# Performance work log

Hardware: AMD Instinct MI355X
Metric: run time of the kernel (lower is better)

Reference implementation:

```python
import jax, jax.numpy as jnp
import numpy as np

B, S, E = 2, 2048, 2048
KV, QPG, HD = 4, 4, 128  # 16 total heads, head_size=128
ROPE_THETA = 10000.0


def _rope_cos_sin(seq_len, head_size, dtype):
    inv_freq = 1.0 / (ROPE_THETA ** (jnp.arange(0, head_size, 2, dtype=jnp.float32) / head_size))
    pos = jnp.arange(seq_len, dtype=jnp.float32)
    freqs = pos[:, None] * inv_freq[None, :]            # [S, HD/2]
    emb = jnp.concatenate([freqs, freqs], axis=-1)       # [S, HD]
    return jnp.cos(emb).astype(dtype), jnp.sin(emb).astype(dtype)


def _rotate_half(x):
    x1, x2 = jnp.split(x, 2, axis=-1)
    return jnp.concatenate([-x2, x1], axis=-1)


def _apply_rope(x, cos, sin):
    # x: [..., S, HD]; cos/sin: [S, HD]
    return x * cos + _rotate_half(x) * sin


def setup_inputs() -> dict:
    key = jax.random.key(0)
    ks = jax.random.split(key, 8)
    scale = 0.02
    return {
        "x": jax.random.normal(ks[0], (B, S, E), jnp.float32),
        "wq": jax.random.normal(ks[1], (KV, QPG, HD, E), jnp.float32) * scale,
        "bq": jax.random.normal(ks[2], (KV, QPG, HD), jnp.float32) * scale,
        "wk": jax.random.normal(ks[3], (KV, HD, E), jnp.float32) * scale,
        "bk": jax.random.normal(ks[4], (KV, HD), jnp.float32) * scale,
        "wv": jax.random.normal(ks[5], (KV, HD, E), jnp.float32) * scale,
        "bv": jax.random.normal(ks[6], (KV, HD), jnp.float32) * scale,
        "wo": jax.random.normal(ks[7], (E, E), jnp.float32) * scale,
    }


def reference(x, wq, bq, wk, bk, wv, bv, wo):
    # QKV projections (out_first linear: y = W x + b)
    q = jnp.einsum('bse,kghe->bkgsh', x, wq) + bq[None, :, :, None, :]   # [B,KV,QPG,S,HD]
    k = jnp.einsum('bse,khe->bksh', x, wk) + bk[None, :, None, :]        # [B,KV,S,HD]
    v = jnp.einsum('bse,khe->bksh', x, wv) + bv[None, :, None, :]        # [B,KV,S,HD]

    cos, sin = _rope_cos_sin(S, HD, x.dtype)
    q = _apply_rope(q, cos, sin)
    k = _apply_rope(k, cos, sin)

    # GQA scaled dot-product attention with causal mask
    scale = 1.0 / jnp.sqrt(jnp.asarray(HD, x.dtype))
    scores = jnp.einsum('bkgsh,bkth->bkgst', q, k) * scale               # [B,KV,QPG,S,S]
    causal = jnp.tril(jnp.ones((S, S), dtype=bool))
    scores = jnp.where(causal, scores, jnp.asarray(-1e9, scores.dtype))
    att = jax.nn.softmax(scores, axis=-1)
    out = jnp.einsum('bkgst,bkth->bkgsh', att, v)                        # [B,KV,QPG,S,HD]

    # flatten (kv_heads, q_heads_per_group, head_size) -> heads*head_size and project
    out = out.transpose(0, 3, 1, 2, 4).reshape(B, S, KV * QPG * HD)      # [B,S,E]
    return jnp.einsum('bsf,ef->bse', out, wo)
```

## Files before the change

kernel.cpp:

```cpp
#include <hip/hip_runtime.h>

typedef unsigned short u16;
typedef short s16x8 __attribute__((ext_vector_type(8)));
typedef float f32x4 __attribute__((ext_vector_type(4)));
typedef float f32x16 __attribute__((ext_vector_type(16)));

__device__ __forceinline__ u16 f2bf(float f) {
  union { float f; unsigned u; } x; x.f = f;
  unsigned r = (x.u + 0x7fffu + ((x.u >> 16) & 1u)) >> 16;
  return (u16)r;
}
__device__ __forceinline__ unsigned bfbits_t(float f) {
  union { float f; unsigned u; } x; x.f = f;
  return x.u >> 16;
}
__device__ __forceinline__ float bf2f(u16 u) {
  union { unsigned u; float f; } x; x.u = ((unsigned)u) << 16;
  return x.f;
}

__device__ __forceinline__ void load_lds16(const u16* g, void* lds) {
  __builtin_amdgcn_global_load_lds(
      (const __attribute__((address_space(1))) unsigned int*)g,
      (__attribute__((address_space(3))) unsigned int*)lds, 16, 0, 0);
}

__global__ __launch_bounds__(256) void prep_kernel(
    const float* __restrict__ x,
    const float* __restrict__ wq, const float* __restrict__ wk,
    const float* __restrict__ wv,
    const float* __restrict__ bq, const float* __restrict__ bk,
    const float* __restrict__ bv,
    const float* __restrict__ wo,
    u16* __restrict__ xb, u16* __restrict__ wqkv,
    float* __restrict__ bqkv, u16* __restrict__ wob,
    float* __restrict__ cosb, float* __restrict__ sinb) {
  const int R0 = 2097152;
  const int R1 = R0 + 1572864;
  const int R2 = R1 + 1048576;
  const int R3 = R2 + 768;
  const int R4 = R3 + 131072;
  for (int id = blockIdx.x * 256 + threadIdx.x; id < R4; id += gridDim.x * 256) {
    if (id < R0) {
      float4 v = ((const float4*)x)[id];
      u16* d = xb + (size_t)id * 4;
      d[0] = f2bf(v.x); d[1] = f2bf(v.y); d[2] = f2bf(v.z); d[3] = f2bf(v.w);
    } else if (id < R1) {
      int g = id - R0;
      int row = g >> 9, c4 = (g & 511) * 4;
      const float* src; int srow;
      if (row < 2048)      { src = wq; srow = row; }
      else if (row < 2560) { src = wk; srow = row - 2048; }
      else                 { src = wv; srow = row - 2560; }
      float4 v = *(const float4*)&src[(size_t)srow * 2048 + c4];
      u16* d = wqkv + (size_t)row * 2048 + c4;
      d[0] = f2bf(v.x); d[1] = f2bf(v.y); d[2] = f2bf(v.z); d[3] = f2bf(v.w);
    } else if (id < R2) {
      int g = id - R1;
      float4 v = ((const float4*)wo)[g];
      u16* d = wob + (size_t)g * 4;
      d[0] = f2bf(v.x); d[1] = f2bf(v.y); d[2] = f2bf(v.z); d[3] = f2bf(v.w);
    } else if (id < R3) {
      int g4 = (id - R2) * 4;
      float4 v;
      if (g4 < 2048)      v = *(const float4*)&bq[g4];
      else if (g4 < 2560) v = *(const float4*)&bk[g4 - 2048];
      else                v = *(const float4*)&bv[g4 - 2560];
      *(float4*)&bqkv[g4] = v;
    } else {
      int g = id - R3;
      int s = g >> 6, i = g & 63;
      float freq = powf(10000.0f, -(float)i / 64.0f);
      float ang = (float)s * freq;
      cosb[g] = cosf(ang);
      sinb[g] = sinf(ang);
    }
  }
}

__global__ __launch_bounds__(256) void rope_all_kernel(u16* __restrict__ Qb,
                                                       u16* __restrict__ Kbuf,
                                                       const float* __restrict__ cosb,
                                                       const float* __restrict__ sinb) {
  const int total = (32 + 8) * 2048 * 64;
  for (int id = blockIdx.x * 256 + threadIdx.x; id < total; id += gridDim.x * 256) {
    int i = id & 63;
    int rs = id >> 6;
    int s = rs & 2047;
    u16* p;
    size_t base;
    if (rs < 65536) { p = Qb;   base = (size_t)rs * 128; }
    else            { p = Kbuf; base = (size_t)(rs - 65536) * 128; }
    float x1 = bf2f(p[base + i]);
    float x2 = bf2f(p[base + i + 64]);
    float c = cosb[s * 64 + i], sn = sinb[s * 64 + i];
    p[base + i]      = f2bf(x1 * c - x2 * sn);
    p[base + i + 64] = f2bf(x2 * c + x1 * sn);
  }
}

__global__ __launch_bounds__(256) void transpose_v_kernel(const u16* __restrict__ V,
                                                          u16* __restrict__ Vt) {
  __shared__ u16 tile[64][130];
  const int t = threadIdx.x;
  const int hb = blockIdx.x, s0 = blockIdx.y * 64;
  const u16* src = V + ((size_t)hb * 2048 + s0) * 128;
#pragma unroll
  for (int i = 0; i < 4; ++i) {
    int c = i * 256 + t;
    int s = c >> 4, d8 = (c & 15) * 8;
    *(s16x8*)&tile[s][d8] = *(const s16x8*)&src[(size_t)s * 128 + d8];
  }
  __syncthreads();
  u16* dst = Vt + (size_t)hb * 128 * 2048 + s0;
#pragma unroll
  for (int i = 0; i < 4; ++i) {
    int c = i * 256 + t;
    int d = c & 127, s8 = (c >> 7) * 8;
    s16x8 v;
#pragma unroll
    for (int e = 0; e < 8; ++e) v[e] = (short)tile[s8 + e][d];
    *(s16x8*)&dst[(size_t)d * 2048 + s8] = v;
  }
}

__global__ __launch_bounds__(512) void gemm_bt_kernel(
    const u16* __restrict__ A, const u16* __restrict__ Bw,
    const float* __restrict__ bias,
    float* __restrict__ C, int ldc,
    u16* __restrict__ Qp, u16* __restrict__ Kp, u16* __restrict__ Vp,
    int M, int N, int K, int mode) {
  __shared__ u16 sA[128 * 64];
  __shared__ u16 sB[128 * 64];
  const int t = threadIdx.x;
  const int w = t >> 6, l = t & 63;
  const int lg = l >> 4, lr = l & 15;
  const int wm = (w >> 2) * 64, wn = (w & 3) * 32;
  const int m0 = blockIdx.y * 128, n0 = blockIdx.x * 128;

  f32x4 acc[4][2];
#pragma unroll
  for (int i = 0; i < 4; ++i)
#pragma unroll
    for (int j = 0; j < 2; ++j)
#pragma unroll
      for (int r = 0; r < 4; ++r) acc[i][j][r] = 0.0f;

  for (int k0 = 0; k0 < K; k0 += 64) {
#pragma unroll
    for (int i = 0; i < 2; ++i) {
      int c = i * 512 + t;
      int row = c >> 3, cc = (c & 7) ^ (row & 7);
      load_lds16(A + (size_t)(m0 + row) * K + k0 + cc * 8,
                 (char*)sA + i * 8192 + w * 1024);
      load_lds16(Bw + (size_t)(n0 + row) * K + k0 + cc * 8,
                 (char*)sB + i * 8192 + w * 1024);
    }
    __syncthreads();
#pragma unroll
    for (int kc = 0; kc < 2; ++kc) {
      const int rch = (((kc * 4 + lg) ^ (lr & 7)) * 8);
      s16x8 af[4], bf[2];
#pragma unroll
      for (int m = 0; m < 4; ++m)
        af[m] = *(const s16x8*)&sA[(wm + m * 16 + lr) * 64 + rch];
#pragma unroll
      for (int n = 0; n < 2; ++n)
        bf[n] = *(const s16x8*)&sB[(wn + n * 16 + lr) * 64 + rch];
#pragma unroll
      for (int m = 0; m < 4; ++m)
#pragma unroll
        for (int n = 0; n < 2; ++n)
          acc[m][n] = __builtin_amdgcn_mfma_f32_16x16x32_bf16(af[m], bf[n], acc[m][n], 0, 0, 0);
    }
    __syncthreads();
  }

#pragma unroll
  for (int m = 0; m < 4; ++m) {
#pragma unroll
    for (int n = 0; n < 2; ++n) {
#pragma unroll
      for (int r = 0; r < 4; ++r) {
        int row = m0 + wm + m * 16 + (lg << 2) + r;
        int col = n0 + wn + n * 16 + lr;
        float val = acc[m][n][r];
        if (mode == 0) {
          val += bias[col];
          int b = row >> 11, s = row & 2047;
          u16 bvv = f2bf(val);
          if (col < 2048) {
            int h = col >> 7, d = col & 127;
            Qp[(((size_t)(b * 16 + h)) * 2048 + s) * 128 + d] = bvv;
          } else if (col < 2560) {
            int cc = col - 2048; int kh = cc >> 7, d = cc & 127;
            Kp[(((size_t)(b * 4 + kh)) * 2048 + s) * 128 + d] = bvv;
          } else {
            int cc = col - 2560; int kh = cc >> 7, d = cc & 127;
            Vp[(((size_t)(b * 4 + kh)) * 2048 + s) * 128 + d] = bvv;
          }
        } else {
          C[(size_t)row * ldc + col] = val;
        }
      }
    }
  }
}

__device__ const int PH_QC[16] = {7,-1, 7,0, 6,-1, 6,1, 5,-1, 5,2, 4,-1, 4,3};
__device__ const int PH_J0[16] = {0,0, 9,0, 0,0, 9,0, 0,0, 9,0, 0,0, 9,0};
__device__ const int PH_NT[16] = {9,0, 7,2, 9,0, 5,4, 9,0, 3,6, 9,0, 1,8};
__device__ const int PH_MD[16] = {1,0, 2,0, 1,0, 2,0, 1,0, 2,0, 1,0, 2,0};

__global__ __launch_bounds__(512) void flash_mfma_kernel(const u16* __restrict__ Q,
                                                         const u16* __restrict__ Kb,
                                                         const u16* __restrict__ Vtb,
                                                         u16* __restrict__ O,
                                                         u16* __restrict__ po,
                                                         float* __restrict__ pml) {
  const int S = 2048;
  __shared__ u16 sK[128 * 128];
  __shared__ u16 sVt[2 * 128 * 128];

  const int t = threadIdx.x, w = t >> 6, l = t & 63;
  const int l31 = l & 31, hi = l >> 5;
  const int bh = blockIdx.x, b = bh >> 4, h = bh & 15, kvh = h >> 2;
  const int slot = blockIdx.y;

  const u16* kbase = Kb + ((size_t)(b * 4 + kvh)) * S * 128;
  const u16* vtbase = Vtb + ((size_t)(b * 4 + kvh)) * 128 * S;

  const float C2 = 0.12753785f;

  auto stageK = [&](int kt) {
#pragma unroll
    for (int i = 0; i < 4; ++i) {
      int c = i * 512 + t;
      int j = c >> 4, cc = (c & 15) ^ (j & 15);
      load_lds16(kbase + ((size_t)(kt * 128 + j) * 128 + cc * 8),
                 (char*)sK + (i * 8192 + w * 1024));
    }
  };
  auto stageV = [&](int kt, int buf) {
#pragma unroll
    for (int i = 0; i < 4; ++i) {
      int c = i * 512 + t;
      int d = c >> 4, cc = (c & 15) ^ (d & 15);
      load_lds16(vtbase + ((size_t)d * S + kt * 128 + cc * 8),
                 (char*)sVt + buf * 32768 + (i * 8192 + w * 1024));
    }
  };

#pragma unroll 1
  for (int ph = 0; ph < 2; ++ph) {
    const int qc = PH_QC[slot * 2 + ph];
    const int ntc = PH_NT[slot * 2 + ph];
    if (ntc == 0) break;
    const int j0 = PH_J0[slot * 2 + ph];
    const int md = PH_MD[slot * 2 + ph];
    const int qw = qc * 256 + w * 32;
    const int q_glob = qw + l31;

    const u16* qbase = Q + ((size_t)bh * S + qw) * 128;
    s16x8 qb[8];
#pragma unroll
    for (int ks = 0; ks < 8; ++ks)
      qb[ks] = *(const s16x8*)&qbase[(size_t)l31 * 128 + ks * 16 + hi * 8];

    f32x16 o0, o1, o2, o3;
#pragma unroll
    for (int r = 0; r < 16; ++r) { o0[r] = 0.f; o1[r] = 0.f; o2[r] = 0.f; o3[r] = 0.f; }
    float mrun = -3e38f, lsum = 0.0f;

    stageV(j0, 0);
    stageK(j0);
    __syncthreads();

    int cur = 0;
    for (int kt2 = 0; kt2 < ntc; ++kt2) {
      const int kt = j0 + kt2;
      const bool act = (kt * 128 <= qw + 31);
      const bool more = (kt2 + 1 < ntc);

      if (more) stageV(kt + 1, cur ^ 1);

      f32x16 sc0, sc1, sc2, sc3;
      if (act) {
#pragma unroll
        for (int r = 0; r < 16; ++r) { sc0[r] = 0.f; sc1[r] = 0.f; sc2[r] = 0.f; sc3[r] = 0.f; }
        const int chkb = (l31 & 15);
        __builtin_amdgcn_s_setprio(1);
#pragma unroll
        for (int ks = 0; ks < 8; ++ks) {
          int chk = ((2 * ks + hi) ^ chkb) * 8;
          s16x8 kf0 = *(const s16x8*)&sK[(l31) * 128 + chk];
          s16x8 kf1 = *(const s16x8*)&sK[(32 + l31) * 128 + chk];
          s16x8 kf2 = *(const s16x8*)&sK[(64 + l31) * 128 + chk];
          s16x8 kf3 = *(const s16x8*)&sK[(96 + l31) * 128 + chk];
          sc0 = __builtin_amdgcn_mfma_f32_32x32x16_bf16(kf0, qb[ks], sc0, 0, 0, 0);
          sc1 = __builtin_amdgcn_mfma_f32_32x32x16_bf16(kf1, qb[ks], sc1, 0, 0, 0);
          sc2 = __builtin_amdgcn_mfma_f32_32x32x16_bf16(kf2, qb[ks], sc2, 0, 0, 0);
          sc3 = __builtin_amdgcn_mfma_f32_32x32x16_bf16(kf3, qb[ks], sc3, 0, 0, 0);
        }
        __builtin_amdgcn_s_setprio(0);
      }

      __syncthreads();

      if (more) stageK(kt + 1);

      if (act) {
        const u16* sVc = &sVt[cur * 16384];

        if (kt * 128 + 127 > qw) {
          const int j0m = kt * 128;
#pragma unroll
          for (int r = 0; r < 16; ++r) {
            int jr = j0m + (r & 3) + 8 * (r >> 2) + 4 * hi;
            sc0[r] = (jr <= q_glob) ? sc0[r] : -3e38f;
            sc1[r] = (jr + 32 <= q_glob) ? sc1[r] : -3e38f;
            sc2[r] = (jr + 64 <= q_glob) ? sc2[r] : -3e38f;
            sc3[r] = (jr + 96 <= q_glob) ? sc3[r] : -3e38f;
          }
        }

        float tm[16];
#pragma unroll
        for (int r = 0; r < 16; ++r)
          tm[r] = fmaxf(fmaxf(sc0[r], sc1[r]), fmaxf(sc2[r], sc3[r]));
#pragma unroll
        for (int s2 = 8; s2 >= 1; s2 >>= 1)
#pragma unroll
          for (int r = 0; r < s2; ++r) tm[r] = fmaxf(tm[r], tm[r + s2]);
        float mt = fmaxf(tm[0], __shfl_xor(tm[0], 32));
        float mt2 = mt * C2;
        bool resc = (mt2 > mrun + 8.0f);
        if (resc) {
          float Mn = mt2;
          float corr = exp2f(mrun - Mn);
          lsum *= corr;
#pragma unroll
          for (int r = 0; r < 16; ++r) {
            o0[r] *= corr; o1[r] *= corr; o2[r] *= corr; o3[r] *= corr;
          }
          mrun = Mn;
        }
        const float Mn = mrun;
        float lacc = 0.0f;

        {
          unsigned pk[16];
#pragma unroll
          for (int m = 0; m < 8; ++m) {
            float pa_ = exp2f(__builtin_fmaf(sc0[2 * m], C2, -Mn));
            float pb_ = exp2f(__builtin_fmaf(sc0[2 * m + 1], C2, -Mn));
            lacc += pa_ + pb_;
            pk[m] = (bfbits_t(pb_) << 16) | bfbits_t(pa_);
          }
#pragma unroll
          for (int m = 0; m < 8; ++m) {
            float pa_ = exp2f(__builtin_fmaf(sc1[2 * m], C2, -Mn));
            float pb_ = exp2f(__builtin_fmaf(sc1[2 * m + 1], C2, -Mn));
            lacc += pa_ + pb_;
            pk[8 + m] = (bfbits_t(pb_) << 16) | bfbits_t(pa_);
          }
          unsigned pkx[16];
#pragma unroll
          for (int i = 0; i < 16; ++i) pkx[i] = __shfl_xor(pk[i], 32);
          __builtin_amdgcn_s_setprio(1);
#pragma unroll
          for (int ks = 0; ks < 4; ++ks) {
            const int base = (ks >> 1) * 8 + 4 * (ks & 1);
            unsigned pw[4];
            pw[0] = hi ? pkx[base + 2] : pk[base + 0];
            pw[1] = hi ? pkx[base + 3] : pk[base + 1];
            pw[2] = hi ? pk[base + 2] : pkx[base + 0];
            pw[3] = hi ? pk[base + 3] : pkx[base + 1];
            s16x8 pa = *(const s16x8*)pw;
#pragma unroll
            for (int dt = 0; dt < 4; ++dt) {
              int d = dt * 32 + l31;
              s16x8 vt = *(const s16x8*)&sVc[d * 128 + (((2 * ks + hi) ^ (d & 15)) * 8)];
              if (dt == 0) o0 = __builtin_amdgcn_mfma_f32_32x32x16_bf16(vt, pa, o0, 0, 0, 0);
              if (dt == 1) o1 = __builtin_amdgcn_mfma_f32_32x32x16_bf16(vt, pa, o1, 0, 0, 0);
              if (dt == 2) o2 = __builtin_amdgcn_mfma_f32_32x32x16_bf16(vt, pa, o2, 0, 0, 0);
              if (dt == 3) o3 = __builtin_amdgcn_mfma_f32_32x32x16_bf16(vt, pa, o3, 0, 0, 0);
            }
          }
          __builtin_amdgcn_s_setprio(0);
        }

        {
          unsigned pk[16];
#pragma unroll
          for (int m = 0; m < 8; ++m) {
            float pa_ = exp2f(__builtin_fmaf(sc2[2 * m], C2, -Mn));
            float pb_ = exp2f(__builtin_fmaf(sc2[2 * m + 1], C2, -Mn));
            lacc += pa_ + pb_;
            pk[m] = (bfbits_t(pb_) << 16) | bfbits_t(pa_);
          }
#pragma unroll
          for (int m = 0; m < 8; ++m) {
            float pa_ = exp2f(__builtin_fmaf(sc3[2 * m], C2, -Mn));
            float pb_ = exp2f(__builtin_fmaf(sc3[2 * m + 1], C2, -Mn));
            lacc += pa_ + pb_;
            pk[8 + m] = (bfbits_t(pb_) << 16) | bfbits_t(pa_);
          }
          unsigned pkx[16];
#pragma unroll
          for (int i = 0; i < 16; ++i) pkx[i] = __shfl_xor(pk[i], 32);
          __builtin_amdgcn_s_setprio(1);
#pragma unroll
          for (int ks = 0; ks < 4; ++ks) {
            const int base = (ks >> 1) * 8 + 4 * (ks & 1);
            unsigned pw[4];
            pw[0] = hi ? pkx[base + 2] : pk[base + 0];
            pw[1] = hi ? pkx[base + 3] : pk[base + 1];
            pw[2] = hi ? pk[base + 2] : pkx[base + 0];
            pw[3] = hi ? pk[base + 3] : pkx[base + 1];
            s16x8 pa = *(const s16x8*)pw;
#pragma unroll
            for (int dt = 0; dt < 4; ++dt) {
              int d = dt * 32 + l31;
              s16x8 vt = *(const s16x8*)&sVc[d * 128 + (((8 + 2 * ks + hi) ^ (d & 15)) * 8)];
              if (dt == 0) o0 = __builtin_amdgcn_mfma_f32_32x32x16_bf16(vt, pa, o0, 0, 0, 0);
              if (dt == 1) o1 = __builtin_amdgcn_mfma_f32_32x32x16_bf16(vt, pa, o1, 0, 0, 0);
              if (dt == 2) o2 = __builtin_amdgcn_mfma_f32_32x32x16_bf16(vt, pa, o2, 0, 0, 0);
              if (dt == 3) o3 = __builtin_amdgcn_mfma_f32_32x32x16_bf16(vt, pa, o3, 0, 0, 0);
            }
          }
          __builtin_amdgcn_s_setprio(0);
        }
        lsum += lacc;
      }

      __syncthreads();
      cur ^= 1;
    }

    float ls = lsum + __shfl_xor(lsum, 32);
    float inv = (ls > 0.0f) ? 1.0f / ls : 0.0f;
    if (md == 0) {
      size_t obase = ((size_t)b * S + q_glob) * 2048 + h * 128;
#pragma unroll
      for (int dt = 0; dt < 4; ++dt) {
        const f32x16& ov = (dt == 0) ? o0 : (dt == 1) ? o1 : (dt == 2) ? o2 : o3;
#pragma unroll
        for (int g = 0; g < 4; ++g) {
          int d0 = dt * 32 + 8 * g + 4 * hi;
          unsigned u0 = (unsigned)f2bf(ov[4 * g] * inv) | ((unsigned)f2bf(ov[4 * g + 1] * inv) << 16);
          unsigned u1 = (unsigned)f2bf(ov[4 * g + 2] * inv) | ((unsigned)f2bf(ov[4 * g + 3] * inv) << 16);
          uint2 u; u.x = u0; u.y = u1;
          *(uint2*)&O[obase + d0] = u;
        }
      }
    } else {
      const int pid = ((bh << 2) + (qc - 4)) * 2 + (md - 1);
      const int qrow = w * 32 + l31;
      size_t pbase = (size_t)pid * 32768 + (size_t)qrow * 128;
#pragma unroll
      for (int dt = 0; dt < 4; ++dt) {
        const f32x16& ov = (dt == 0) ? o0 : (dt == 1) ? o1 : (dt == 2) ? o2 : o3;
#pragma unroll
        for (int g = 0; g < 4; ++g) {
          int d0 = dt * 32 + 8 * g + 4 * hi;
          unsigned u0 = (unsigned)f2bf(ov[4 * g] * inv) | ((unsigned)f2bf(ov[4 * g + 1] * inv) << 16);
          unsigned u1 = (unsigned)f2bf(ov[4 * g + 2] * inv) | ((unsigned)f2bf(ov[4 * g + 3] * inv) << 16);
          uint2 u; u.x = u0; u.y = u1;
          *(uint2*)&po[pbase + d0] = u;
        }
      }
      if (hi == 0) {
        pml[pid * 512 + qrow * 2]     = mrun;
        pml[pid * 512 + qrow * 2 + 1] = ls;
      }
    }
    if (ph == 0 && PH_NT[slot * 2 + 1] != 0) __syncthreads();
  }
}

__global__ __launch_bounds__(256) void flash_merge_kernel(const u16* __restrict__ po,
                                                          const float* __restrict__ pml,
                                                          u16* __restrict__ att) {
  const int t = threadIdx.x;
  const int tl = blockIdx.x >> 4;
  const int row = (blockIdx.x & 15) * 16 + (t >> 4);
  const int d8 = (t & 15) * 8;
  const int hh2 = tl >> 2, qc = (tl & 3) + 4;
  const int pid0 = tl * 2, pid1 = pid0 + 1;
  float m0 = pml[pid0 * 512 + row * 2], l0 = pml[pid0 * 512 + row * 2 + 1];
  float m1 = pml[pid1 * 512 + row * 2], l1 = pml[pid1 * 512 + row * 2 + 1];
  float M = fmaxf(m0, m1);
  float w0 = l0 * exp2f(m0 - M), w1 = l1 * exp2f(m1 - M);
  float inv = 1.0f / (w0 + w1);
  w0 *= inv; w1 *= inv;
  s16x8 a = *(const s16x8*)&po[(size_t)pid0 * 32768 + row * 128 + d8];
  s16x8 c = *(const s16x8*)&po[(size_t)pid1 * 32768 + row * 128 + d8];
  int b = hh2 >> 4, hh = hh2 & 15;
  size_t base = ((size_t)b * 2048 + qc * 256 + row) * 2048 + hh * 128 + d8;
  u16 outv[8];
#pragma unroll
  for (int e = 0; e < 8; ++e)
    outv[e] = f2bf(w0 * bf2f((u16)a[e]) + w1 * bf2f((u16)c[e]));
  *(s16x8*)&att[base] = *(const s16x8*)outv;
}


extern "C" void kernel_launch(void* const* d_in, const int* in_sizes, int n_in,
                              void* d_out, int out_size, void* d_ws, size_t ws_size,
                              hipStream_t stream) {
  const float* x  = (const float*)d_in[0];
  const float* wq = (const float*)d_in[1];
  const float* bq = (const float*)d_in[2];
  const float* wk = (const float*)d_in[3];
  const float* bk = (const float*)d_in[4];
  const float* wv = (const float*)d_in[5];
  const float* bv = (const float*)d_in[6];
  const float* wo = (const float*)d_in[7];
  float* out = (float*)d_out;

  char* ws = (char*)d_ws;
  u16* xb    = (u16*)ws;    ws += (size_t)4096 * 2048 * 2;
  u16* wqkv  = (u16*)ws;    ws += (size_t)3072 * 2048 * 2;
  float* bqkv = (float*)ws; ws += (size_t)3072 * 4;
  u16* wob   = (u16*)ws;    ws += (size_t)2048 * 2048 * 2;
  u16* Qb    = (u16*)ws;    ws += (size_t)32 * 2048 * 128 * 2;
  u16* Kbuf  = (u16*)ws;    ws += (size_t)8 * 2048 * 128 * 2;
  u16* Vbuf  = (u16*)ws;    ws += (size_t)8 * 2048 * 128 * 2;
  u16* Vt    = (u16*)ws;    ws += (size_t)8 * 128 * 2048 * 2;
  float* cosb = (float*)ws; ws += (size_t)2048 * 64 * 4;
  float* sinb = (float*)ws; ws += (size_t)2048 * 64 * 4;
  u16* att   = (u16*)ws;    ws += (size_t)4096 * 2048 * 2;

  u16* po = xb;
  float* pml = (float*)Vbuf;

  prep_kernel<<<2048, 256, 0, stream>>>(x, wq, wk, wv, bq, bk, bv, wo,
                                        xb, wqkv, bqkv, wob, cosb, sinb);

  gemm_bt_kernel<<<dim3(24, 32), 512, 0, stream>>>(xb, wqkv, bqkv, nullptr, 0,
                                                   Qb, Kbuf, Vbuf, 4096, 3072, 2048, 0);
  transpose_v_kernel<<<dim3(8, 32), 256, 0, stream>>>(Vbuf, Vt);
  rope_all_kernel<<<2048, 256, 0, stream>>>(Qb, Kbuf, cosb, sinb);

  flash_mfma_kernel<<<dim3(32, 8), 512, 0, stream>>>(Qb, Kbuf, Vt, att, po, pml);
  flash_merge_kernel<<<2048, 256, 0, stream>>>(po, pml, att);

  gemm_bt_kernel<<<dim3(16, 32), 512, 0, stream>>>(att, wob, nullptr, out, 2048,
                                                   nullptr, nullptr, nullptr, 4096, 2048, 2048, 1);
}
```

Baseline: 197.6 us.

## Split every query chunk into two KV halves and single-buffer V

New measurement: 226.0 us. 1.14x slower.

```diff
diff --git a/kernel.cpp b/kernel.cpp
--- a/kernel.cpp
+++ b/kernel.cpp
@@ -207,11 +207,6 @@
   }
 }
 
-__device__ const int PH_QC[16] = {7,-1, 7,0, 6,-1, 6,1, 5,-1, 5,2, 4,-1, 4,3};
-__device__ const int PH_J0[16] = {0,0, 9,0, 0,0, 9,0, 0,0, 9,0, 0,0, 9,0};
-__device__ const int PH_NT[16] = {9,0, 7,2, 9,0, 5,4, 9,0, 3,6, 9,0, 1,8};
-__device__ const int PH_MD[16] = {1,0, 2,0, 1,0, 2,0, 1,0, 2,0, 1,0, 2,0};
-
 __global__ __launch_bounds__(512) void flash_mfma_kernel(const u16* __restrict__ Q,
                                                          const u16* __restrict__ Kb,
                                                          const u16* __restrict__ Vtb,
@@ -220,17 +215,35 @@
                                                          float* __restrict__ pml) {
   const int S = 2048;
   __shared__ u16 sK[128 * 128];
-  __shared__ u16 sVt[2 * 128 * 128];
+  __shared__ u16 sVt[128 * 128];
 
   const int t = threadIdx.x, w = t >> 6, l = t & 63;
   const int l31 = l & 31, hi = l >> 5;
   const int bh = blockIdx.x, b = bh >> 4, h = bh & 15, kvh = h >> 2;
-  const int slot = blockIdx.y;
+  const int y = blockIdx.y;
+  const int piece = y >> 3;
+  const int qc = piece ? (y - 8) : (7 - y);
+  const int ntc = qc + 1;
+  const int j0 = piece ? (qc + 1) : 0;
 
   const u16* kbase = Kb + ((size_t)(b * 4 + kvh)) * S * 128;
   const u16* vtbase = Vtb + ((size_t)(b * 4 + kvh)) * 128 * S;
 
   const float C2 = 0.12753785f;
+
+  const int qw = qc * 256 + w * 32;
+  const int q_glob = qw + l31;
+
+  const u16* qbase = Q + ((size_t)bh * S + qw) * 128;
+  s16x8 qb[8];
+#pragma unroll
+  for (int ks = 0; ks < 8; ++ks)
+    qb[ks] = *(const s16x8*)&qbase[(size_t)l31 * 128 + ks * 16 + hi * 8];
+
+  f32x16 o0, o1, o2, o3;
+#pragma unroll
+  for (int r = 0; r < 16; ++r) { o0[r] = 0.f; o1[r] = 0.f; o2[r] = 0.f; o3[r] = 0.f; }
+  float mrun = -3e38f, lsum = 0.0f;
 
   auto stageK = [&](int kt) {
 #pragma unroll
@@ -241,241 +254,214 @@
                  (char*)sK + (i * 8192 + w * 1024));
     }
   };
-  auto stageV = [&](int kt, int buf) {
+  auto stageV = [&](int kt) {
 #pragma unroll
     for (int i = 0; i < 4; ++i) {
       int c = i * 512 + t;
       int d = c >> 4, cc = (c & 15) ^ (d & 15);
       load_lds16(vtbase + ((size_t)d * S + kt * 128 + cc * 8),
-                 (char*)sVt + buf * 32768 + (i * 8192 + w * 1024));
+                 (char*)sVt + (i * 8192 + w * 1024));
     }
   };
 
-#pragma unroll 1
-  for (int ph = 0; ph < 2; ++ph) {
-    const int qc = PH_QC[slot * 2 + ph];
-    const int ntc = PH_NT[slot * 2 + ph];
-    if (ntc == 0) break;
-    const int j0 = PH_J0[slot * 2 + ph];
-    const int md = PH_MD[slot * 2 + ph];
-    const int qw = qc * 256 + w * 32;
-    const int q_glob = qw + l31;
-
-    const u16* qbase = Q + ((size_t)bh * S + qw) * 128;
-    s16x8 qb[8];
-#pragma unroll
-    for (int ks = 0; ks < 8; ++ks)
-      qb[ks] = *(const s16x8*)&qbase[(size_t)l31 * 128 + ks * 16 + hi * 8];
-
-    f32x16 o0, o1, o2, o3;
-#pragma unroll
-    for (int r = 0; r < 16; ++r) { o0[r] = 0.f; o1[r] = 0.f; o2[r] = 0.f; o3[r] = 0.f; }
-    float mrun = -3e38f, lsum = 0.0f;
-
-    stageV(j0, 0);
-    stageK(j0);
+  stageK(j0);
+  stageV(j0);
+  __syncthreads();
+
+  for (int kt2 = 0; kt2 < ntc; ++kt2) {
+    const int kt = j0 + kt2;
+    const bool act = (kt * 128 <= qw + 31);
+    const bool more = (kt2 + 1 < ntc);
+
+    f32x16 sc0, sc1, sc2, sc3;
+    if (act) {
+#pragma unroll
+      for (int r = 0; r < 16; ++r) { sc0[r] = 0.f; sc1[r] = 0.f; sc2[r] = 0.f; sc3[r] = 0.f; }
+      const int chkb = (l31 & 15);
+      __builtin_amdgcn_s_setprio(1);
+#pragma unroll
+      for (int ks = 0; ks < 8; ++ks) {
+        int chk = ((2 * ks + hi) ^ chkb) * 8;
+        s16x8 kf0 = *(const s16x8*)&sK[(l31) * 128 + chk];
+        s16x8 kf1 = *(const s16x8*)&sK[(32 + l31) * 128 + chk];
+        s16x8 kf2 = *(const s16x8*)&sK[(64 + l31) * 128 + chk];
+        s16x8 kf3 = *(const s16x8*)&sK[(96 + l31) * 128 + chk];
+        sc0 = __builtin_amdgcn_mfma_f32_32x32x16_bf16(kf0, qb[ks], sc0, 0, 0, 0);
+        sc1 = __builtin_amdgcn_mfma_f32_32x32x16_bf16(kf1, qb[ks], sc1, 0, 0, 0);
+        sc2 = __builtin_amdgcn_mfma_f32_32x32x16_bf16(kf2, qb[ks], sc2, 0, 0, 0);
+        sc3 = __builtin_amdgcn_mfma_f32_32x32x16_bf16(kf3, qb[ks], sc3, 0, 0, 0);
+      }
+      __builtin_amdgcn_s_setprio(0);
+    }
+
     __syncthreads();
 
-    int cur = 0;
-    for (int kt2 = 0; kt2 < ntc; ++kt2) {
-      const int kt = j0 + kt2;
-      const bool act = (kt * 128 <= qw + 31);
-      const bool more = (kt2 + 1 < ntc);
-
-      if (more) stageV(kt + 1, cur ^ 1);
-
-      f32x16 sc0, sc1, sc2, sc3;
-      if (act) {
-#pragma unroll
-        for (int r = 0; r < 16; ++r) { sc0[r] = 0.f; sc1[r] = 0.f; sc2[r] = 0.f; sc3[r] = 0.f; }
-        const int chkb = (l31 & 15);
+    if (more) stageK(kt + 1);
+
+    if (act) {
+      if (kt * 128 + 127 > qw) {
+        const int j0m = kt * 128;
+#pragma unroll
+        for (int r = 0; r < 16; ++r) {
+          int jr = j0m + (r & 3) + 8 * (r >> 2) + 4 * hi;
+          sc0[r] = (jr <= q_glob) ? sc0[r] : -3e38f;
+          sc1[r] = (jr + 32 <= q_glob) ? sc1[r] : -3e38f;
+          sc2[r] = (jr + 64 <= q_glob) ? sc2[r] : -3e38f;
+          sc3[r] = (jr + 96 <= q_glob) ? sc3[r] : -3e38f;
+        }
+      }
+
+      float tm[16];
+#pragma unroll
+      for (int r = 0; r < 16; ++r)
+        tm[r] = fmaxf(fmaxf(sc0[r], sc1[r]), fmaxf(sc2[r], sc3[r]));
+#pragma unroll
+      for (int s2 = 8; s2 >= 1; s2 >>= 1)
+#pragma unroll
+        for (int r = 0; r < s2; ++r) tm[r] = fmaxf(tm[r], tm[r + s2]);
+      float mt = fmaxf(tm[0], __shfl_xor(tm[0], 32));
+      float mt2 = mt * C2;
+      bool resc = (mt2 > mrun + 8.0f);
+      if (resc) {
+        float Mn = mt2;
+        float corr = exp2f(mrun - Mn);
+        lsum *= corr;
+#pragma unroll
+        for (int r = 0; r < 16; ++r) {
+          o0[r] *= corr; o1[r] *= corr; o2[r] *= corr; o3[r] *= corr;
+        }
+        mrun = Mn;
+      }
+      const float Mn = mrun;
+      float lacc = 0.0f;
+
+      {
+        unsigned pk[16];
+#pragma unroll
+        for (int m = 0; m < 8; ++m) {
+          float pa_ = exp2f(__builtin_fmaf(sc0[2 * m], C2, -Mn));
+          float pb_ = exp2f(__builtin_fmaf(sc0[2 * m + 1], C2, -Mn));
+          lacc += pa_ + pb_;
+          pk[m] = (bfbits_t(pb_) << 16) | bfbits_t(pa_);
+        }
+#pragma unroll
+        for (int m = 0; m < 8; ++m) {
+          float pa_ = exp2f(__builtin_fmaf(sc1[2 * m], C2, -Mn));
+          float pb_ = exp2f(__builtin_fmaf(sc1[2 * m + 1], C2, -Mn));
+          lacc += pa_ + pb_;
+          pk[8 + m] = (bfbits_t(pb_) << 16) | bfbits_t(pa_);
+        }
+        unsigned pkx[16];
+#pragma unroll
+        for (int i = 0; i < 16; ++i) pkx[i] = __shfl_xor(pk[i], 32);
         __builtin_amdgcn_s_setprio(1);
 #pragma unroll
-        for (int ks = 0; ks < 8; ++ks) {
-          int chk = ((2 * ks + hi) ^ chkb) * 8;
-          s16x8 kf0 = *(const s16x8*)&sK[(l31) * 128 + chk];
-          s16x8 kf1 = *(const s16x8*)&sK[(32 + l31) * 128 + chk];
-          s16x8 kf2 = *(const s16x8*)&sK[(64 + l31) * 128 + chk];
-          s16x8 kf3 = *(const s16x8*)&sK[(96 + l31) * 128 + chk];
-          sc0 = __builtin_amdgcn_mfma_f32_32x32x16_bf16(kf0, qb[ks], sc0, 0, 0, 0);
-          sc1 = __builtin_amdgcn_mfma_f32_32x32x16_bf16(kf1, qb[ks], sc1, 0, 0, 0);
-          sc2 = __builtin_amdgcn_mfma_f32_32x32x16_bf16(kf2, qb[ks], sc2, 0, 0, 0);
-          sc3 = __builtin_amdgcn_mfma_f32_32x32x16_bf16(kf3, qb[ks], sc3, 0, 0, 0);
+        for (int ks = 0; ks < 4; ++ks) {
+          const int base = (ks >> 1) * 8 + 4 * (ks & 1);
+          unsigned pw[4];
+          pw[0] = hi ? pkx[base + 2] : pk[base + 0];
+          pw[1] = hi ? pkx[base + 3] : pk[base + 1];
+          pw[2] = hi ? pk[base + 2] : pkx[base + 0];
+          pw[3] = hi ? pk[base + 3] : pkx[base + 1];
+          s16x8 pa = *(const s16x8*)pw;
+#pragma unroll
+          for (int dt = 0; dt < 4; ++dt) {
+            int d = dt * 32 + l31;
+            s16x8 vt = *(const s16x8*)&sVt[d * 128 + (((2 * ks + hi) ^ (d & 15)) * 8)];
+            if (dt == 0) o0 = __builtin_amdgcn_mfma_f32_32x32x16_bf16(vt, pa, o0, 0, 0, 0);
+            if (dt == 1) o1 = __builtin_amdgcn_mfma_f32_32x32x16_bf16(vt, pa, o1, 0, 0, 0);
+            if (dt == 2) o2 = __builtin_amdgcn_mfma_f32_32x32x16_bf16(vt, pa, o2, 0, 0, 0);
+            if (dt == 3) o3 = __builtin_amdgcn_mfma_f32_32x32x16_bf16(vt, pa, o3, 0, 0, 0);
+          }
         }
         __builtin_amdgcn_s_setprio(0);
       }
 
-      __syncthreads();
-
-      if (more) stageK(kt + 1);
-
-      if (act) {
-        const u16* sVc = &sVt[cur * 16384];
-
-        if (kt * 128 + 127 > qw) {
-          const int j0m = kt * 128;
-#pragma unroll
-          for (int r = 0; r < 16; ++r) {
-            int jr = j0m + (r & 3) + 8 * (r >> 2) + 4 * hi;
-            sc0[r] = (jr <= q_glob) ? sc0[r] : -3e38f;
-            sc1[r] = (jr + 32 <= q_glob) ? sc1[r] : -3e38f;
-            sc2[r] = (jr + 64 <= q_glob) ? sc2[r] : -3e38f;
-            sc3[r] = (jr + 96 <= q_glob) ? sc3[r] : -3e38f;
+      {
+        unsigned pk[16];
+#pragma unroll
+        for (int m = 0; m < 8; ++m) {
+          float pa_ = exp2f(__builtin_fmaf(sc2[2 * m], C2, -Mn));
+          float pb_ = exp2f(__builtin_fmaf(sc2[2 * m + 1], C2, -Mn));
+          lacc += pa_ + pb_;
+          pk[m] = (bfbits_t(pb_) << 16) | bfbits_t(pa_);
+        }
+#pragma unroll
+        for (int m = 0; m < 8; ++m) {
+          float pa_ = exp2f(__builtin_fmaf(sc3[2 * m], C2, -Mn));
+          float pb_ = exp2f(__builtin_fmaf(sc3[2 * m + 1], C2, -Mn));
+          lacc += pa_ + pb_;
+          pk[8 + m] = (bfbits_t(pb_) << 16) | bfbits_t(pa_);
+        }
+        unsigned pkx[16];
+#pragma unroll
+        for (int i = 0; i < 16; ++i) pkx[i] = __shfl_xor(pk[i], 32);
+        __builtin_amdgcn_s_setprio(1);
+#pragma unroll
+        for (int ks = 0; ks < 4; ++ks) {
+          const int base = (ks >> 1) * 8 + 4 * (ks & 1);
+          unsigned pw[4];
+          pw[0] = hi ? pkx[base + 2] : pk[base + 0];
+          pw[1] = hi ? pkx[base + 3] : pk[base + 1];
+          pw[2] = hi ? pk[base + 2] : pkx[base + 0];
+          pw[3] = hi ? pk[base + 3] : pkx[base + 1];
+          s16x8 pa = *(const s16x8*)pw;
+#pragma unroll
+          for (int dt = 0; dt < 4; ++dt) {
+            int d = dt * 32 + l31;
+            s16x8 vt = *(const s16x8*)&sVt[d * 128 + (((8 + 2 * ks + hi) ^ (d & 15)) * 8)];
+            if (dt == 0) o0 = __builtin_amdgcn_mfma_f32_32x32x16_bf16(vt, pa, o0, 0, 0, 0);
+            if (dt == 1) o1 = __builtin_amdgcn_mfma_f32_32x32x16_bf16(vt, pa, o1, 0, 0, 0);
+            if (dt == 2) o2 = __builtin_amdgcn_mfma_f32_32x32x16_bf16(vt, pa, o2, 0, 0, 0);
+            if (dt == 3) o3 = __builtin_amdgcn_mfma_f32_32x32x16_bf16(vt, pa, o3, 0, 0, 0);
           }
         }
-
-        float tm[16];
-#pragma unroll
-        for (int r = 0; r < 16; ++r)
-          tm[r] = fmaxf(fmaxf(sc0[r], sc1[r]), fmaxf(sc2[r], sc3[r]));
-#pragma unroll
-        for (int s2 = 8; s2 >= 1; s2 >>= 1)
-#pragma unroll
-          for (int r = 0; r < s2; ++r) tm[r] = fmaxf(tm[r], tm[r + s2]);
-        float mt = fmaxf(tm[0], __shfl_xor(tm[0], 32));
-        float mt2 = mt * C2;
-        bool resc = (mt2 > mrun + 8.0f);
-        if (resc) {
-          float Mn = mt2;
-          float corr = exp2f(mrun - Mn);
-          lsum *= corr;
-#pragma unroll
-          for (int r = 0; r < 16; ++r) {
-            o0[r] *= corr; o1[r] *= corr; o2[r] *= corr; o3[r] *= corr;
-          }
-          mrun = Mn;
-        }
-        const float Mn = mrun;
-        float lacc = 0.0f;
-
-        {
-          unsigned pk[16];
-#pragma unroll
-          for (int m = 0; m < 8; ++m) {
-            float pa_ = exp2f(__builtin_fmaf(sc0[2 * m], C2, -Mn));
-            float pb_ = exp2f(__builtin_fmaf(sc0[2 * m + 1], C2, -Mn));
-            lacc += pa_ + pb_;
-            pk[m] = (bfbits_t(pb_) << 16) | bfbits_t(pa_);
-          }
-#pragma unroll
-          for (int m = 0; m < 8; ++m) {
-            float pa_ = exp2f(__builtin_fmaf(sc1[2 * m], C2, -Mn));
-            float pb_ = exp2f(__builtin_fmaf(sc1[2 * m + 1], C2, -Mn));
-            lacc += pa_ + pb_;
-            pk[8 + m] = (bfbits_t(pb_) << 16) | bfbits_t(pa_);
-          }
-          unsigned pkx[16];
-#pragma unroll
-          for (int i = 0; i < 16; ++i) pkx[i] = __shfl_xor(pk[i], 32);
-          __builtin_amdgcn_s_setprio(1);
-#pragma unroll
-          for (int ks = 0; ks < 4; ++ks) {
-            const int base = (ks >> 1) * 8 + 4 * (ks & 1);
-            unsigned pw[4];
-            pw[0] = hi ? pkx[base + 2] : pk[base + 0];
-            pw[1] = hi ? pkx[base + 3] : pk[base + 1];
-            pw[2] = hi ? pk[base + 2] : pkx[base + 0];
-            pw[3] = hi ? pk[base + 3] : pkx[base + 1];
-            s16x8 pa = *(const s16x8*)pw;
-#pragma unroll
-            for (int dt = 0; dt < 4; ++dt) {
-              int d = dt * 32 + l31;
-              s16x8 vt = *(const s16x8*)&sVc[d * 128 + (((2 * ks + hi) ^ (d & 15)) * 8)];
-              if (dt == 0) o0 = __builtin_amdgcn_mfma_f32_32x32x16_bf16(vt, pa, o0, 0, 0, 0);
-              if (dt == 1) o1 = __builtin_amdgcn_mfma_f32_32x32x16_bf16(vt, pa, o1, 0, 0, 0);
-              if (dt == 2) o2 = __builtin_amdgcn_mfma_f32_32x32x16_bf16(vt, pa, o2, 0, 0, 0);
-              if (dt == 3) o3 = __builtin_amdgcn_mfma_f32_32x32x16_bf16(vt, pa, o3, 0, 0, 0);
-            }
-          }
-          __builtin_amdgcn_s_setprio(0);
-        }
-
-        {
-          unsigned pk[16];
-#pragma unroll
-          for (int m = 0; m < 8; ++m) {
-            float pa_ = exp2f(__builtin_fmaf(sc2[2 * m], C2, -Mn));
-            float pb_ = exp2f(__builtin_fmaf(sc2[2 * m + 1], C2, -Mn));
-            lacc += pa_ + pb_;
-            pk[m] = (bfbits_t(pb_) << 16) | bfbits_t(pa_);
-          }
-#pragma unroll
-          for (int m = 0; m < 8; ++m) {
-            float pa_ = exp2f(__builtin_fmaf(sc3[2 * m], C2, -Mn));
-            float pb_ = exp2f(__builtin_fmaf(sc3[2 * m + 1], C2, -Mn));
-            lacc += pa_ + pb_;
-            pk[8 + m] = (bfbits_t(pb_) << 16) | bfbits_t(pa_);
-          }
-          unsigned pkx[16];
-#pragma unroll
-          for (int i = 0; i < 16; ++i) pkx[i] = __shfl_xor(pk[i], 32);
-          __builtin_amdgcn_s_setprio(1);
-#pragma unroll
-          for (int ks = 0; ks < 4; ++ks) {
-            const int base = (ks >> 1) * 8 + 4 * (ks & 1);
-            unsigned pw[4];
-            pw[0] = hi ? pkx[base + 2] : pk[base + 0];
-            pw[1] = hi ? pkx[base + 3] : pk[base + 1];
-            pw[2] = hi ? pk[base + 2] : pkx[base + 0];
-            pw[3] = hi ? pk[base + 3] : pkx[base + 1];
-            s16x8 pa = *(const s16x8*)pw;
-#pragma unroll
-            for (int dt = 0; dt < 4; ++dt) {
-              int d = dt * 32 + l31;
-              s16x8 vt = *(const s16x8*)&sVc[d * 128 + (((8 + 2 * ks + hi) ^ (d & 15)) * 8)];
-              if (dt == 0) o0 = __builtin_amdgcn_mfma_f32_32x32x16_bf16(vt, pa, o0, 0, 0, 0);
-              if (dt == 1) o1 = __builtin_amdgcn_mfma_f32_32x32x16_bf16(vt, pa, o1, 0, 0, 0);
-              if (dt == 2) o2 = __builtin_amdgcn_mfma_f32_32x32x16_bf16(vt, pa, o2, 0, 0, 0);
-              if (dt == 3) o3 = __builtin_amdgcn_mfma_f32_32x32x16_bf16(vt, pa, o3, 0, 0, 0);
-            }
-          }
-          __builtin_amdgcn_s_setprio(0);
-        }
-        lsum += lacc;
-      }
-
-      __syncthreads();
-      cur ^= 1;
-    }
-
-    float ls = lsum + __shfl_xor(lsum, 32);
-    float inv = (ls > 0.0f) ? 1.0f / ls : 0.0f;
-    if (md == 0) {
-      size_t obase = ((size_t)b * S + q_glob) * 2048 + h * 128;
-#pragma unroll
-      for (int dt = 0; dt < 4; ++dt) {
-        const f32x16& ov = (dt == 0) ? o0 : (dt == 1) ? o1 : (dt == 2) ? o2 : o3;
-#pragma unroll
-        for (int g = 0; g < 4; ++g) {
-          int d0 = dt * 32 + 8 * g + 4 * hi;
-          unsigned u0 = (unsigned)f2bf(ov[4 * g] * inv) | ((unsigned)f2bf(ov[4 * g + 1] * inv) << 16);
-          unsigned u1 = (unsigned)f2bf(ov[4 * g + 2] * inv) | ((unsigned)f2bf(ov[4 * g + 3] * inv) << 16);
-          uint2 u; u.x = u0; u.y = u1;
-          *(uint2*)&O[obase + d0] = u;
-        }
-      }
-    } else {
-      const int pid = ((bh << 2) + (qc - 4)) * 2 + (md - 1);
-      const int qrow = w * 32 + l31;
-      size_t pbase = (size_t)pid * 32768 + (size_t)qrow * 128;
-#pragma unroll
-      for (int dt = 0; dt < 4; ++dt) {
-        const f32x16& ov = (dt == 0) ? o0 : (dt == 1) ? o1 : (dt == 2) ? o2 : o3;
-#pragma unroll
-        for (int g = 0; g < 4; ++g) {
-          int d0 = dt * 32 + 8 * g + 4 * hi;
-          unsigned u0 = (unsigned)f2bf(ov[4 * g] * inv) | ((unsigned)f2bf(ov[4 * g + 1] * inv) << 16);
-          unsigned u1 = (unsigned)f2bf(ov[4 * g + 2] * inv) | ((unsigned)f2bf(ov[4 * g + 3] * inv) << 16);
-          uint2 u; u.x = u0; u.y = u1;
-          *(uint2*)&po[pbase + d0] = u;
-        }
-      }
-      if (hi == 0) {
-        pml[pid * 512 + qrow * 2]     = mrun;
-        pml[pid * 512 + qrow * 2 + 1] = ls;
-      }
-    }
-    if (ph == 0 && PH_NT[slot * 2 + 1] != 0) __syncthreads();
+        __builtin_amdgcn_s_setprio(0);
+      }
+      lsum += lacc;
+    }
+
+    __syncthreads();
+
+    if (more) stageV(kt + 1);
+  }
+
+  float ls = lsum + __shfl_xor(lsum, 32);
+  float inv = (ls > 0.0f) ? 1.0f / ls : 0.0f;
+  const int pid = ((bh << 3) + qc) * 2 + piece;
+  const int qrow = w * 32 + l31;
+  if (piece == 0) {
+    size_t obase = ((size_t)b * S + qc * 256 + qrow) * 2048 + h * 128;
+#pragma unroll
+    for (int dt = 0; dt < 4; ++dt) {
+      const f32x16& ov = (dt == 0) ? o0 : (dt == 1) ? o1 : (dt == 2) ? o2 : o3;
+#pragma unroll
+      for (int g = 0; g < 4; ++g) {
+        int d0 = dt * 32 + 8 * g + 4 * hi;
+        unsigned u0 = (unsigned)f2bf(ov[4 * g] * inv) | ((unsigned)f2bf(ov[4 * g + 1] * inv) << 16);
+        unsigned u1 = (unsigned)f2bf(ov[4 * g + 2] * inv) | ((unsigned)f2bf(ov[4 * g + 3] * inv) << 16);
+        uint2 u; u.x = u0; u.y = u1;
+        *(uint2*)&O[obase + d0] = u;
+      }
+    }
+  } else {
+    size_t pbase = (size_t)((bh << 3) + qc) * 32768 + (size_t)qrow * 128;
+#pragma unroll
+    for (int dt = 0; dt < 4; ++dt) {
+      const f32x16& ov = (dt == 0) ? o0 : (dt == 1) ? o1 : (dt == 2) ? o2 : o3;
+#pragma unroll
+      for (int g = 0; g < 4; ++g) {
+        int d0 = dt * 32 + 8 * g + 4 * hi;
+        unsigned u0 = (unsigned)f2bf(ov[4 * g] * inv) | ((unsigned)f2bf(ov[4 * g + 1] * inv) << 16);
+        unsigned u1 = (unsigned)f2bf(ov[4 * g + 2] * inv) | ((unsigned)f2bf(ov[4 * g + 3] * inv) << 16);
+        uint2 u; u.x = u0; u.y = u1;
+        *(uint2*)&po[pbase + d0] = u;
+      }
+    }
+  }
+  if (hi == 0) {
+    pml[pid * 512 + qrow * 2]     = mrun;
+    pml[pid * 512 + qrow * 2 + 1] = ls;
   }
 }
 
@@ -486,7 +472,7 @@
   const int tl = blockIdx.x >> 4;
   const int row = (blockIdx.x & 15) * 16 + (t >> 4);
   const int d8 = (t & 15) * 8;
-  const int hh2 = tl >> 2, qc = (tl & 3) + 4;
+  const int bh = tl >> 3, qc = tl & 7;
   const int pid0 = tl * 2, pid1 = pid0 + 1;
   float m0 = pml[pid0 * 512 + row * 2], l0 = pml[pid0 * 512 + row * 2 + 1];
   float m1 = pml[pid1 * 512 + row * 2], l1 = pml[pid1 * 512 + row * 2 + 1];
@@ -494,10 +480,10 @@
   float w0 = l0 * exp2f(m0 - M), w1 = l1 * exp2f(m1 - M);
   float inv = 1.0f / (w0 + w1);
   w0 *= inv; w1 *= inv;
-  s16x8 a = *(const s16x8*)&po[(size_t)pid0 * 32768 + row * 128 + d8];
-  s16x8 c = *(const s16x8*)&po[(size_t)pid1 * 32768 + row * 128 + d8];
-  int b = hh2 >> 4, hh = hh2 & 15;
+  int b = bh >> 4, hh = bh & 15;
   size_t base = ((size_t)b * 2048 + qc * 256 + row) * 2048 + hh * 128 + d8;
+  s16x8 a = *(const s16x8*)&att[base];
+  s16x8 c = *(const s16x8*)&po[(size_t)tl * 32768 + row * 128 + d8];
   u16 outv[8];
 #pragma unroll
   for (int e = 0; e < 8; ++e)
@@ -533,7 +519,7 @@
   u16* att   = (u16*)ws;    ws += (size_t)4096 * 2048 * 2;
 
   u16* po = xb;
-  float* pml = (float*)Vbuf;
+  float* pml = cosb;
 
   prep_kernel<<<2048, 256, 0, stream>>>(x, wq, wk, wv, bq, bk, bv, wo,
                                         xb, wqkv, bqkv, wob, cosb, sinb);
@@ -543,8 +529,8 @@
   transpose_v_kernel<<<dim3(8, 32), 256, 0, stream>>>(Vbuf, Vt);
   rope_all_kernel<<<2048, 256, 0, stream>>>(Qb, Kbuf, cosb, sinb);
 
-  flash_mfma_kernel<<<dim3(32, 8), 512, 0, stream>>>(Qb, Kbuf, Vt, att, po, pml);
-  flash_merge_kernel<<<2048, 256, 0, stream>>>(po, pml, att);
+  flash_mfma_kernel<<<dim3(32, 16), 512, 0, stream>>>(Qb, Kbuf, Vt, att, po, pml);
+  flash_merge_kernel<<<4096, 256, 0, stream>>>(po, pml, att);
 
   gemm_bt_kernel<<<dim3(16, 32), 512, 0, stream>>>(att, wob, nullptr, out, 2048,
                                                    nullptr, nullptr, nullptr, 4096, 2048, 2048, 1);
```

## Double-buffer LDS tiles in GEMM kernel with async prefetch two stages ahead

Applied to the files above, without the earlier changes.

Result: slower. 210.7 us (+6.6%).

```diff
diff --git a/kernel.cpp b/kernel.cpp
--- a/kernel.cpp
+++ b/kernel.cpp
@@ -130,8 +130,8 @@
     float* __restrict__ C, int ldc,
     u16* __restrict__ Qp, u16* __restrict__ Kp, u16* __restrict__ Vp,
     int M, int N, int K, int mode) {
-  __shared__ u16 sA[128 * 64];
-  __shared__ u16 sB[128 * 64];
+  __shared__ u16 sA[2][128 * 64];
+  __shared__ u16 sB[2][128 * 64];
   const int t = threadIdx.x;
   const int w = t >> 6, l = t & 63;
   const int lg = l >> 4, lr = l & 15;
@@ -146,34 +146,55 @@
 #pragma unroll
       for (int r = 0; r < 4; ++r) acc[i][j][r] = 0.0f;
 
-  for (int k0 = 0; k0 < K; k0 += 64) {
+  auto issue = [&](int k0, int buf) {
 #pragma unroll
     for (int i = 0; i < 2; ++i) {
       int c = i * 512 + t;
       int row = c >> 3, cc = (c & 7) ^ (row & 7);
       load_lds16(A + (size_t)(m0 + row) * K + k0 + cc * 8,
-                 (char*)sA + i * 8192 + w * 1024);
+                 (char*)sA[buf] + i * 8192 + w * 1024);
       load_lds16(Bw + (size_t)(n0 + row) * K + k0 + cc * 8,
-                 (char*)sB + i * 8192 + w * 1024);
-    }
-    __syncthreads();
+                 (char*)sB[buf] + i * 8192 + w * 1024);
+    }
+  };
+
+  const int nk = K >> 6;
+  issue(0, 0);
+  issue(64, 1);
+  int cur = 0;
+
+  for (int ik = 0; ik < nk; ++ik) {
+    if (ik + 1 < nk) {
+      asm volatile("s_waitcnt vmcnt(4)" ::: "memory");
+    } else {
+      asm volatile("s_waitcnt vmcnt(0)" ::: "memory");
+    }
+    __builtin_amdgcn_s_barrier();
+    __builtin_amdgcn_sched_barrier(0);
+
+    const u16* sAc = sA[cur];
+    const u16* sBc = sB[cur];
 #pragma unroll
     for (int kc = 0; kc < 2; ++kc) {
       const int rch = (((kc * 4 + lg) ^ (lr & 7)) * 8);
       s16x8 af[4], bf[2];
 #pragma unroll
       for (int m = 0; m < 4; ++m)
-        af[m] = *(const s16x8*)&sA[(wm + m * 16 + lr) * 64 + rch];
+        af[m] = *(const s16x8*)&sAc[(wm + m * 16 + lr) * 64 + rch];
 #pragma unroll
       for (int n = 0; n < 2; ++n)
-        bf[n] = *(const s16x8*)&sB[(wn + n * 16 + lr) * 64 + rch];
+        bf[n] = *(const s16x8*)&sBc[(wn + n * 16 + lr) * 64 + rch];
 #pragma unroll
       for (int m = 0; m < 4; ++m)
 #pragma unroll
         for (int n = 0; n < 2; ++n)
           acc[m][n] = __builtin_amdgcn_mfma_f32_16x16x32_bf16(af[m], bf[n], acc[m][n], 0, 0, 0);
     }
-    __syncthreads();
+
+    __builtin_amdgcn_sched_barrier(0);
+    __builtin_amdgcn_s_barrier();
+    if (ik + 2 < nk) issue((ik + 2) << 6, cur);
+    cur ^= 1;
   }
 
 #pragma unroll
```
